# Kernel tuning notes

Hardware: AMD Instinct MI355X
Metric: run time of the kernel (lower is better)

Reference implementation:

```python
import jax, jax.numpy as jnp
import numpy as np

EMBED_DIM = 1024
N_HEADS = 16
HEAD_DIM = EMBED_DIM // N_HEADS
B, N = 4, 2048


def setup_inputs() -> dict:
    key = jax.random.key(0)
    k1, k2, k3, k4, k5 = jax.random.split(key, 5)
    x = jax.random.normal(k1, (B, N, EMBED_DIM), dtype=jnp.float32)
    # Per-head kqv Linear weights stacked: torch Linear(embed_dim, 3*head_dim)
    # torch stores weight as [out, in]; we store transposed [in, out] per head.
    scale = 1.0 / np.sqrt(EMBED_DIM)
    W_kqv = jax.random.uniform(k2, (N_HEADS, EMBED_DIM, 3 * HEAD_DIM), dtype=jnp.float32, minval=-scale, maxval=scale)
    b_kqv = jax.random.uniform(k3, (N_HEADS, 3 * HEAD_DIM), dtype=jnp.float32, minval=-scale, maxval=scale)
    W_proj = jax.random.uniform(k4, (EMBED_DIM, EMBED_DIM), dtype=jnp.float32, minval=-scale, maxval=scale)
    b_proj = jax.random.uniform(k5, (EMBED_DIM,), dtype=jnp.float32, minval=-scale, maxval=scale)
    return {"x": x, "W_kqv": W_kqv, "b_kqv": b_kqv, "W_proj": W_proj, "b_proj": b_proj}


def reference(x, W_kqv, b_kqv, W_proj, b_proj):
    Bx, Nx, D = x.shape
    H = W_kqv.shape[0]
    hd = W_kqv.shape[2] // 3
    # All per-head kqv projections at once: [B, H, N, 3*hd]
    kqv = jnp.einsum('bnd,hde->bhne', x, W_kqv) + b_kqv[None, :, None, :]
    # chunk order in source is (k, q, v)
    k, q, v = jnp.split(kqv, 3, axis=-1)
    # scores scaled by sqrt(head_dim) (D1 in attention_scores is head dim)
    scores = jnp.einsum('bhqd,bhkd->bhqk', q, k) / jnp.sqrt(jnp.float32(hd))
    causal = jnp.tril(jnp.ones((Nx, Nx), dtype=bool))  # [N, N]
    scores = jnp.where(causal[None, None, :, :], scores, -jnp.inf)
    attn = jax.nn.softmax(scores, axis=-1)
    sa = jnp.einsum('bhqk,bhkd->bhqd', attn, v)  # [B, H, N, hd]
    # concat heads along feature dim (head order preserved)
    sa = sa.transpose(0, 2, 1, 3).reshape(Bx, Nx, H * hd)
    # output projection: torch Linear with weight [out, in] -> y = sa @ W^T + b;
    # here W_proj is stored as [in, out]
    return sa @ W_proj + b_proj
```

## Files before the change

### kernel.cpp

```cpp
#include <hip/hip_runtime.h>
#include <math.h>

#define EMBED   1024
#define NHEADS  16
#define HD      64
#define BATCH   4
#define SEQ     2048
#define MROWS   (BATCH*SEQ)
#define NKV     8388608ull

typedef short short8 __attribute__((ext_vector_type(8)));
typedef float floatx4 __attribute__((ext_vector_type(4)));

__device__ __forceinline__ unsigned short f2b(float f) {
    union { float f; unsigned u; } v; v.f = f;
    unsigned r = v.u + 0x7FFFu + ((v.u >> 16) & 1u);
    return (unsigned short)(r >> 16);
}
__device__ __forceinline__ unsigned short f2b_fast(float f) {
    union { float f; unsigned u; } v; v.f = f;
    return (unsigned short)((v.u + 0x8000u) >> 16);
}

#define GLDS16(gp, lp) __builtin_amdgcn_global_load_lds( \
    (const __attribute__((address_space(1))) unsigned int*)(gp), \
    (__attribute__((address_space(3))) unsigned int*)(lp), 16, 0, 0)

__global__ __launch_bounds__(256) void convert_x(
    const float* __restrict__ x, unsigned short* __restrict__ x16)
{
    size_t idx = ((size_t)blockIdx.x * 256 + threadIdx.x) * 8;
    float4 a = *(const float4*)(x + idx);
    float4 b = *(const float4*)(x + idx + 4);
    ushort4 u0, u1;
    u0.x = f2b(a.x); u0.y = f2b(a.y); u0.z = f2b(a.z); u0.w = f2b(a.w);
    u1.x = f2b(b.x); u1.y = f2b(b.y); u1.z = f2b(b.z); u1.w = f2b(b.w);
    *(ushort4*)(x16 + idx) = u0;
    *(ushort4*)(x16 + idx + 4) = u1;
}

__global__ __launch_bounds__(256) void prep_wkqv(
    const float* __restrict__ Wk, unsigned short* __restrict__ Wt)
{
    __shared__ float tile[32][33];
    const int h = blockIdx.z;
    const int k0 = blockIdx.x * 32, e0 = blockIdx.y * 32;
    const float* inh = Wk + (size_t)h * 1024 * 192;
    const int tx = threadIdx.x & 31, ty = threadIdx.x >> 5;
    #pragma unroll
    for (int i = 0; i < 4; i++)
        tile[ty + i * 8][tx] = inh[(size_t)(k0 + ty + i * 8) * 192 + e0 + tx];
    __syncthreads();
    #pragma unroll
    for (int i = 0; i < 4; i++) {
        int e = e0 + ty + i * 8;
        int cp = (e >> 6) * 1024 + h * 64 + (e & 63);
        Wt[(size_t)cp * 1024 + k0 + tx] = f2b(tile[tx][ty + i * 8]);
    }
}

__global__ __launch_bounds__(256) void transpose_w(
    const float* __restrict__ in, unsigned short* __restrict__ outp, int R, int C)
{
    __shared__ float tile[32][33];
    const int r0 = blockIdx.x * 32, c0 = blockIdx.y * 32;
    const int tx = threadIdx.x & 31, ty = threadIdx.x >> 5;
    #pragma unroll
    for (int i = 0; i < 4; i++)
        tile[ty + i * 8][tx] = in[(size_t)(r0 + ty + i * 8) * C + c0 + tx];
    __syncthreads();
    #pragma unroll
    for (int i = 0; i < 4; i++)
        outp[(size_t)(c0 + ty + i * 8) * R + r0 + tx] = f2b(tile[tx][ty + i * 8]);
}

__global__ __launch_bounds__(512, 2) void gemm_kqv(
    const unsigned short* __restrict__ A,
    const unsigned short* __restrict__ Bt,
    const float* __restrict__ bk,
    unsigned short* __restrict__ Kb16,
    unsigned short* __restrict__ Qb16,
    unsigned short* __restrict__ Vt16)
{
    __shared__ unsigned short smem[65536];

    const int mt = blockIdx.x;
    const int ct = blockIdx.y;
    const int t = threadIdx.x;
    const int wave = t >> 6, lane = t & 63;
    const int lr = lane & 15, quad = lane >> 4;
    const int wr = wave >> 2, wc = wave & 3;
    const int row0 = mt * 256, col0 = ct * 256;
    const int swz8 = ((lane & 7) ^ ((lane >> 3) & 7)) * 8;
    const int c0 = ((quad) ^ (lr & 7)) * 8;
    const int c1 = ((4 + quad) ^ (lr & 7)) * 8;

    floatx4 acc[8][4];
    #pragma unroll
    for (int m = 0; m < 8; m++)
        #pragma unroll
        for (int n = 0; n < 4; n++) acc[m][n] = (floatx4){0.f, 0.f, 0.f, 0.f};

#define STG(G, R0, KC, L) do { \
    _Pragma("unroll") \
    for (int i_ = 0; i_ < 2; i_++) { \
        int rl_ = i_ * 64 + wave * 8 + (lane >> 3); \
        GLDS16((G) + (size_t)((R0) + rl_) * 1024 + (KC) + swz8, \
               (L) + rl_ * 64 + (lane & 7) * 8); \
    } } while (0)

    STG(A,  row0,       0,  smem);
    STG(A,  row0 + 128, 0,  smem + 8192);
    STG(Bt, col0,       0,  smem + 16384);
    STG(Bt, col0 + 128, 0,  smem + 16384 + 8192);
    STG(Bt, col0,       64, smem + 32768 + 16384);
    STG(Bt, col0 + 128, 64, smem + 32768 + 16384 + 8192);
    asm volatile("s_waitcnt vmcnt(4)" ::: "memory");
    __builtin_amdgcn_s_barrier();

    #pragma unroll 2
    for (int j = 0; j < 16; ++j) {
        unsigned short* Ab = smem + (j & 1) * 32768;
        unsigned short* Bb = Ab + 16384;
        unsigned short* An = smem + ((j + 1) & 1) * 32768;
        const unsigned short* pA = Ab + (wr * 128 + lr) * 64;
        const unsigned short* pB = Bb + (wc * 64 + lr) * 64;

        short8 b0[4], b1[4];

        {
            short8 af[4];
            #pragma unroll
            for (int m = 0; m < 4; m++) af[m] = *(const short8*)(pA + m * 1024 + c0);
            #pragma unroll
            for (int n = 0; n < 4; n++) b0[n] = *(const short8*)(pB + n * 1024 + c0);
            if (j < 15) STG(A, row0, (j + 1) * 64, An);
            __builtin_amdgcn_s_barrier();
            asm volatile("s_waitcnt lgkmcnt(0)" ::: "memory");
            __builtin_amdgcn_s_setprio(1);
            #pragma unroll
            for (int m = 0; m < 4; m++)
                #pragma unroll
                for (int n = 0; n < 4; n++)
                    acc[m][n] = __builtin_amdgcn_mfma_f32_16x16x32_bf16(af[m], b0[n], acc[m][n], 0, 0, 0);
            __builtin_amdgcn_s_setprio(0);
            __builtin_amdgcn_s_barrier();
        }
        {
            short8 af[4];
            #pragma unroll
            for (int m = 0; m < 4; m++) af[m] = *(const short8*)(pA + (m + 4) * 1024 + c0);
            #pragma unroll
            for (int n = 0; n < 4; n++) b1[n] = *(const short8*)(pB + n * 1024 + c1);
            if (j < 15) STG(A, row0 + 128, (j + 1) * 64, An + 8192);
            __builtin_amdgcn_s_barrier();
            asm volatile("s_waitcnt lgkmcnt(0)" ::: "memory");
            __builtin_amdgcn_s_setprio(1);
            #pragma unroll
            for (int m = 0; m < 4; m++)
                #pragma unroll
                for (int n = 0; n < 4; n++)
                    acc[m + 4][n] = __builtin_amdgcn_mfma_f32_16x16x32_bf16(af[m], b0[n], acc[m + 4][n], 0, 0, 0);
            __builtin_amdgcn_s_setprio(0);
            __builtin_amdgcn_s_barrier();
        }
        {
            short8 af[4];
            #pragma unroll
            for (int m = 0; m < 4; m++) af[m] = *(const short8*)(pA + m * 1024 + c1);
            if (j < 14) STG(Bt, col0, (j + 2) * 64, Bb);
            __builtin_amdgcn_s_barrier();
            asm volatile("s_waitcnt lgkmcnt(0)" ::: "memory");
            __builtin_amdgcn_s_setprio(1);
            #pragma unroll
            for (int m = 0; m < 4; m++)
                #pragma unroll
                for (int n = 0; n < 4; n++)
                    acc[m][n] = __builtin_amdgcn_mfma_f32_16x16x32_bf16(af[m], b1[n], acc[m][n], 0, 0, 0);
            __builtin_amdgcn_s_setprio(0);
            __builtin_amdgcn_s_barrier();
        }
        {
            short8 af[4];
            #pragma unroll
            for (int m = 0; m < 4; m++) af[m] = *(const short8*)(pA + (m + 4) * 1024 + c1);
            if (j < 14) STG(Bt, col0 + 128, (j + 2) * 64, Bb + 8192);
            __builtin_amdgcn_s_barrier();
            asm volatile("s_waitcnt lgkmcnt(0)" ::: "memory");
            __builtin_amdgcn_s_setprio(1);
            #pragma unroll
            for (int m = 0; m < 4; m++)
                #pragma unroll
                for (int n = 0; n < 4; n++)
                    acc[m + 4][n] = __builtin_amdgcn_mfma_f32_16x16x32_bf16(af[m], b1[n], acc[m + 4][n], 0, 0, 0);
            __builtin_amdgcn_s_setprio(0);
            if (j < 14)       asm volatile("s_waitcnt vmcnt(4)" ::: "memory");
            else if (j == 14) asm volatile("s_waitcnt vmcnt(0)" ::: "memory");
            __builtin_amdgcn_s_barrier();
        }
    }
#undef STG

    unsigned short* W = smem + wave * 8192;
    const int sec = ct >> 2;
    const int h = ((ct & 3) << 2) + wc;
    const int bidx = mt >> 3;
    const int rbase = ((mt * 256) & 2047) + wr * 128;

    float bias[4];
    #pragma unroll
    for (int n = 0; n < 4; n++) bias[n] = bk[h * 192 + sec * 64 + n * 16 + lr];

    if (sec < 2) {
        const float scl = (sec == 1) ? (0.125f * 1.44269504089f) : 1.0f;
        #pragma unroll
        for (int m = 0; m < 8; m++)
            #pragma unroll
            for (int n = 0; n < 4; n++) {
                int es = (n * 16 + lr) ^ (quad << 4);
                #pragma unroll
                for (int r = 0; r < 4; r++)
                    W[(m * 16 + quad * 4 + r) * 64 + es] = f2b((acc[m][n][r] + bias[n]) * scl);
            }
        __syncthreads();
        unsigned short* dst = ((sec == 0) ? Kb16 : Qb16)
                              + ((size_t)(bidx * 16 + h) * 2048 + rbase) * 64;
        const int rrow = lane >> 3, chunk = lane & 7;
        #pragma unroll
        for (int p = 0; p < 16; p++) {
            int row = p * 8 + rrow;
            int ch = chunk ^ (((row >> 2) & 3) << 1);
            *(float4*)(dst + (size_t)row * 64 + chunk * 8) =
                *(const float4*)(W + row * 64 + ch * 8);
        }
    } else {
        #pragma unroll
        for (int m = 0; m < 8; m++)
            #pragma unroll
            for (int n = 0; n < 4; n++) {
                int e = n * 16 + lr;
                ushort4 pk;
                pk.x = f2b(acc[m][n][0] + bias[n]);
                pk.y = f2b(acc[m][n][1] + bias[n]);
                pk.z = f2b(acc[m][n][2] + bias[n]);
                pk.w = f2b(acc[m][n][3] + bias[n]);
                int mp = m ^ (lr & 7);
                *(ushort4*)(W + e * 128 + mp * 16 + quad * 4) = pk;
            }
        __syncthreads();
        unsigned short* dstV = Vt16 + (size_t)(bidx * 16 + h) * 64 * 2048 + rbase;
        const int ev = lane >> 4, chunkR = lane & 15;
        #pragma unroll
        for (int p = 0; p < 16; p++) {
            int e = p * 4 + ev;
            int ch = chunkR ^ ((e & 7) << 1);
            *(float4*)(dstV + (size_t)e * 2048 + chunkR * 8) =
                *(const float4*)(W + e * 128 + ch * 8);
        }
    }
}

__global__ __launch_bounds__(256, 2) void attn_mfma(
    const unsigned short* __restrict__ Kb,
    const unsigned short* __restrict__ Qb,
    const unsigned short* __restrict__ Vt,
    unsigned short* __restrict__ sa)
{
    const int bx = blockIdx.x;
    const int bh = blockIdx.y;
    const int b = bh >> 4, h = bh & 15;
    const int wave = threadIdx.x >> 6;
    const int lane = threadIdx.x & 63;
    const int lr = lane & 15, quad = lane >> 4;
    const int qt_[2] = {bx, 15 - bx};

    __shared__ unsigned short Ks[64 * 64];
    __shared__ unsigned short Vs[64 * 64];
    __shared__ unsigned short Ps[4][2][16 * 72];

    const unsigned short* Kbh = Kb + (size_t)bh * 2048 * 64;
    const unsigned short* Vbh = Vt + (size_t)bh * 64 * 2048;
    const unsigned short* Qbh = Qb + (size_t)bh * 2048 * 64;

    short8 qf[2][2][2];
    #pragma unroll
    for (int tt = 0; tt < 2; tt++)
        #pragma unroll
        for (int s = 0; s < 2; s++) {
            const unsigned short* qp = Qbh +
                (size_t)(qt_[tt] * 128 + wave * 32 + s * 16 + lr) * 64 + quad * 8;
            qf[tt][s][0] = *(const short8*)(qp);
            qf[tt][s][1] = *(const short8*)(qp + 32);
        }

    floatx4 O[2][2][4];
    float ls[2][2][4];
    #pragma unroll
    for (int tt = 0; tt < 2; tt++)
        #pragma unroll
        for (int s = 0; s < 2; s++) {
            #pragma unroll
            for (int d = 0; d < 4; d++) O[tt][s][d] = (floatx4){0.f, 0.f, 0.f, 0.f};
            #pragma unroll
            for (int r = 0; r < 4; r++) ls[tt][s][r] = 0.f;
        }

    const int r_local = lane >> 3, cc = lane & 7;
    const int swz = cc ^ r_local;
    const int whalf = wave >> 1;

    const int ktmax = 2 * qt_[1] + 1;
    for (int kt = 0; kt <= ktmax; kt++) {
        const int k0 = kt * 64;
        __syncthreads();
        #pragma unroll
        for (int j = 0; j < 2; j++) {
            int R = wave * 16 + j * 8 + r_local;
            GLDS16(Kbh + (size_t)(k0 + R) * 64 + swz * 8, Ks + (wave * 16 + j * 8) * 64 + lane * 8);
            GLDS16(Vbh + (size_t)R * 2048 + k0 + swz * 8, Vs + (wave * 16 + j * 8) * 64 + lane * 8);
        }
        __syncthreads();

        #pragma unroll
        for (int tt = 0; tt < 2; tt++) {
            const int qt2 = qt_[tt];
            const int lim = 2 * qt2 + whalf;
            if (kt > lim) continue;

            floatx4 S[2][4];
            #pragma unroll
            for (int s = 0; s < 2; s++)
                #pragma unroll
                for (int a = 0; a < 4; a++) S[s][a] = (floatx4){0.f, 0.f, 0.f, 0.f};
            #pragma unroll
            for (int c = 0; c < 2; c++)
                #pragma unroll
                for (int a = 0; a < 4; a++) {
                    int R = a * 16 + lr;
                    short8 kf = *(const short8*)(Ks + R * 64 + (((c * 4 + quad) ^ (lr & 7)) * 8));
                    #pragma unroll
                    for (int s = 0; s < 2; s++)
                        S[s][a] = __builtin_amdgcn_mfma_f32_16x16x32_bf16(qf[tt][s][c], kf, S[s][a], 0, 0, 0);
                }

            if (kt == lim) {
                #pragma unroll
                for (int s = 0; s < 2; s++)
                    #pragma unroll
                    for (int a = 0; a < 4; a++) {
                        int col = k0 + a * 16 + lr;
                        #pragma unroll
                        for (int r = 0; r < 4; r++) {
                            int grow = qt2 * 128 + wave * 32 + s * 16 + quad * 4 + r;
                            if (col > grow) S[s][a][r] = -INFINITY;
                        }
                    }
            }

            #pragma unroll
            for (int s = 0; s < 2; s++)
                #pragma unroll
                for (int a = 0; a < 4; a++)
                    #pragma unroll
                    for (int r = 0; r < 4; r++) {
                        float p = __builtin_amdgcn_exp2f(S[s][a][r]);
                        ls[tt][s][r] += p;
                        Ps[wave][s][(quad * 4 + r) * 72 + a * 16 + lr] = f2b_fast(p);
                    }

            short8 pa[2][2];
            #pragma unroll
            for (int s = 0; s < 2; s++)
                #pragma unroll
                for (int c = 0; c < 2; c++)
                    pa[s][c] = *(const short8*)(Ps[wave][s] + lr * 72 + c * 32 + quad * 8);

            #pragma unroll
            for (int c = 0; c < 2; c++)
                #pragma unroll
                for (int d = 0; d < 4; d++) {
                    int R = d * 16 + lr;
                    short8 vf = *(const short8*)(Vs + R * 64 + (((c * 4 + quad) ^ (lr & 7)) * 8));
                    #pragma unroll
                    for (int s = 0; s < 2; s++)
                        O[tt][s][d] = __builtin_amdgcn_mfma_f32_16x16x32_bf16(pa[s][c], vf, O[tt][s][d], 0, 0, 0);
                }
        }
    }

    #pragma unroll
    for (int tt = 0; tt < 2; tt++)
        #pragma unroll
        for (int s = 0; s < 2; s++)
            #pragma unroll
            for (int r = 0; r < 4; r++) {
                float sm = ls[tt][s][r];
                sm += __shfl_xor(sm, 1);
                sm += __shfl_xor(sm, 2);
                sm += __shfl_xor(sm, 4);
                sm += __shfl_xor(sm, 8);
                float inv = 1.0f / sm;
                size_t base = ((size_t)(b * 2048 + qt_[tt] * 128 + wave * 32 + s * 16 + quad * 4 + r)) * 1024
                              + h * 64 + lr;
                #pragma unroll
                for (int d = 0; d < 4; d++)
                    sa[base + d * 16] = f2b(O[tt][s][d][r] * inv);
            }
}

__global__ __launch_bounds__(256) void gemm_proj(
    const unsigned short* __restrict__ A,
    const unsigned short* __restrict__ Bt,
    const float* __restrict__ bp,
    float* __restrict__ out)
{
    __shared__ unsigned short smem[16384];
    unsigned short* As = smem;
    unsigned short* Bs = smem + 8192;

    const int mt = blockIdx.x;
    const int ct = blockIdx.y;
    const int t = threadIdx.x;
    const int wave = t >> 6, lane = t & 63;
    const int lr = lane & 15, quad = lane >> 4;
    const int wm = wave >> 1, wn = wave & 1;
    const int row0 = mt * 128, col0 = ct * 128;
    const int sr = lane >> 3, sc = lane & 7;

    floatx4 acc[4][4];
    #pragma unroll
    for (int a = 0; a < 4; a++)
        #pragma unroll
        for (int n = 0; n < 4; n++) acc[a][n] = (floatx4){0.f, 0.f, 0.f, 0.f};

    for (int k0 = 0; k0 < 1024; k0 += 64) {
        __syncthreads();
        #pragma unroll
        for (int i = 0; i < 4; i++) {
            int q = wave + i * 4;
            GLDS16(A  + (size_t)(row0 + q * 8 + sr) * 1024 + k0 + sc * 8, As + q * 512);
            GLDS16(Bt + (size_t)(col0 + q * 8 + sr) * 1024 + k0 + sc * 8, Bs + q * 512);
        }
        __syncthreads();
        #pragma unroll
        for (int kc = 0; kc < 2; kc++) {
            short8 af[4], bf[4];
            #pragma unroll
            for (int i = 0; i < 4; i++) {
                af[i] = *(const short8*)(As + (wm * 64 + i * 16 + lr) * 64 + kc * 32 + quad * 8);
                bf[i] = *(const short8*)(Bs + (wn * 64 + i * 16 + lr) * 64 + kc * 32 + quad * 8);
            }
            #pragma unroll
            for (int a = 0; a < 4; a++)
                #pragma unroll
                for (int n = 0; n < 4; n++)
                    acc[a][n] = __builtin_amdgcn_mfma_f32_16x16x32_bf16(af[a], bf[n], acc[a][n], 0, 0, 0);
        }
    }

    float bias[4]; int cols[4];
    #pragma unroll
    for (int n = 0; n < 4; n++) {
        cols[n] = col0 + wn * 64 + n * 16 + lr;
        bias[n] = bp[cols[n]];
    }
    #pragma unroll
    for (int a = 0; a < 4; a++) {
        #pragma unroll
        for (int n = 0; n < 4; n++) {
            #pragma unroll
            for (int r = 0; r < 4; r++) {
                int m = row0 + wm * 64 + a * 16 + quad * 4 + r;
                out[(size_t)m * 1024 + cols[n]] = acc[a][n][r] + bias[n];
            }
        }
    }
}

extern "C" void kernel_launch(void* const* d_in, const int* in_sizes, int n_in,
                              void* d_out, int out_size, void* d_ws, size_t ws_size,
                              hipStream_t stream) {
    const float* x  = (const float*)d_in[0];
    const float* Wk = (const float*)d_in[1];
    const float* bk = (const float*)d_in[2];
    const float* Wp = (const float*)d_in[3];
    const float* bp = (const float*)d_in[4];
    float* out = (float*)d_out;

    unsigned short* Kb16 = (unsigned short*)d_ws;
    unsigned short* Qb16 = Kb16 + NKV;
    unsigned short* Vt16 = Qb16 + NKV;
    unsigned short* sa16 = Vt16 + NKV;
    unsigned short* x16  = sa16 + 8388608ull;
    unsigned short* Wt   = x16  + 8388608ull;
    unsigned short* Wpt  = Wt   + 3145728ull;

    convert_x<<<4096, 256, 0, stream>>>(x, x16);
    prep_wkqv<<<dim3(32, 6, 16), 256, 0, stream>>>(Wk, Wt);
    transpose_w<<<dim3(32, 32, 1), 256, 0, stream>>>(Wp, Wpt, 1024, 1024);
    gemm_kqv<<<dim3(32, 12), 512, 0, stream>>>(x16, Wt, bk, Kb16, Qb16, Vt16);
    attn_mfma<<<dim3(8, 64), 256, 0, stream>>>(Kb16, Qb16, Vt16, sa16);
    gemm_proj<<<dim3(64, 8), 256, 0, stream>>>(sa16, Wpt, bp, out);
}
```

Before: 254.1 us.

## Share pipelined 128x256 GEMM mainloop between KQV and output projection

Factors a swizzled, double-buffered 128x256 bf16 MFMA mainloop into a shared device function. gemm_kqv switches from 256x256 tiles to 128x256 tiles, doubling its grid from 384 to 768 blocks, which should fill the compute units more evenly. gemm_proj drops its simple single-buffered 128x128 loop for the pipelined 128x256 loop with 512 threads. The trade-off is less reuse of each B tile per block in gemm_kqv, and gemm_proj now has only 256 blocks.

```diff
diff --git a/kernel.cpp b/kernel.cpp
--- a/kernel.cpp
+++ b/kernel.cpp
@@ -74,6 +74,91 @@
         outp[(size_t)(c0 + ty + i * 8) * R + r0 + tx] = f2b(tile[tx][ty + i * 8]);
 }
 
+__device__ __forceinline__ void mainloop_128x256(
+    const unsigned short* __restrict__ Ag,
+    const unsigned short* __restrict__ Bg,
+    unsigned short* smem,
+    int row0, int col0, floatx4 (&acc)[4][4])
+{
+    const int t = threadIdx.x;
+    const int wave = t >> 6, lane = t & 63;
+    const int lr = lane & 15, quad = lane >> 4;
+    const int wr = wave >> 2, wc = wave & 3;
+    const int swz8 = ((lane & 7) ^ ((lane >> 3) & 7)) * 8;
+    const int c0 = (quad ^ (lr & 7)) * 8;
+    const int c1 = ((4 + quad) ^ (lr & 7)) * 8;
+
+    #pragma unroll
+    for (int m = 0; m < 4; m++)
+        #pragma unroll
+        for (int n = 0; n < 4; n++) acc[m][n] = (floatx4){0.f, 0.f, 0.f, 0.f};
+
+#define STG(G, R0, KC, L) do { \
+    _Pragma("unroll") \
+    for (int i_ = 0; i_ < 2; i_++) { \
+        int rl_ = i_ * 64 + wave * 8 + (lane >> 3); \
+        GLDS16((G) + (size_t)((R0) + rl_) * 1024 + (KC) + swz8, \
+               (L) + rl_ * 64 + (lane & 7) * 8); \
+    } } while (0)
+
+    STG(Ag, row0,       0,  smem);
+    STG(Bg, col0,       0,  smem + 8192);
+    STG(Bg, col0 + 128, 0,  smem + 16384);
+    STG(Bg, col0,       64, smem + 24576 + 8192);
+    STG(Bg, col0 + 128, 64, smem + 24576 + 16384);
+    asm volatile("s_waitcnt vmcnt(4)" ::: "memory");
+    __builtin_amdgcn_s_barrier();
+
+    #pragma unroll 2
+    for (int j = 0; j < 16; ++j) {
+        unsigned short* Ab = smem + (j & 1) * 24576;
+        unsigned short* Bb = Ab + 8192;
+        unsigned short* An = smem + ((j + 1) & 1) * 24576;
+        const unsigned short* pA = Ab + (wr * 64 + lr) * 64;
+        const unsigned short* pB = Bb + (wc * 64 + lr) * 64;
+
+        short8 af0[4], af1[4], b0[4], b1[4];
+
+        #pragma unroll
+        for (int m = 0; m < 4; m++) af0[m] = *(const short8*)(pA + m * 1024 + c0);
+        #pragma unroll
+        for (int n = 0; n < 4; n++) b0[n] = *(const short8*)(pB + n * 1024 + c0);
+        #pragma unroll
+        for (int n = 0; n < 4; n++) b1[n] = *(const short8*)(pB + n * 1024 + c1);
+        if (j < 15) STG(Ag, row0, (j + 1) * 64, An);
+        __builtin_amdgcn_s_barrier();
+        asm volatile("s_waitcnt lgkmcnt(0)" ::: "memory");
+        __builtin_amdgcn_s_setprio(1);
+        #pragma unroll
+        for (int m = 0; m < 4; m++)
+            #pragma unroll
+            for (int n = 0; n < 4; n++)
+                acc[m][n] = __builtin_amdgcn_mfma_f32_16x16x32_bf16(af0[m], b0[n], acc[m][n], 0, 0, 0);
+        __builtin_amdgcn_s_setprio(0);
+        __builtin_amdgcn_s_barrier();
+
+        #pragma unroll
+        for (int m = 0; m < 4; m++) af1[m] = *(const short8*)(pA + m * 1024 + c1);
+        if (j < 14) {
+            STG(Bg, col0,       (j + 2) * 64, Bb);
+            STG(Bg, col0 + 128, (j + 2) * 64, Bb + 8192);
+        }
+        __builtin_amdgcn_s_barrier();
+        asm volatile("s_waitcnt lgkmcnt(0)" ::: "memory");
+        __builtin_amdgcn_s_setprio(1);
+        #pragma unroll
+        for (int m = 0; m < 4; m++)
+            #pragma unroll
+            for (int n = 0; n < 4; n++)
+                acc[m][n] = __builtin_amdgcn_mfma_f32_16x16x32_bf16(af1[m], b1[n], acc[m][n], 0, 0, 0);
+        __builtin_amdgcn_s_setprio(0);
+        if (j < 14)       asm volatile("s_waitcnt vmcnt(4)" ::: "memory");
+        else if (j == 14) asm volatile("s_waitcnt vmcnt(0)" ::: "memory");
+        __builtin_amdgcn_s_barrier();
+    }
+#undef STG
+}
+
 __global__ __launch_bounds__(512, 2) void gemm_kqv(
     const unsigned short* __restrict__ A,
     const unsigned short* __restrict__ Bt,
@@ -82,130 +167,25 @@
     unsigned short* __restrict__ Qb16,
     unsigned short* __restrict__ Vt16)
 {
-    __shared__ unsigned short smem[65536];
+    __shared__ unsigned short smem[49152];
 
     const int mt = blockIdx.x;
     const int ct = blockIdx.y;
+    const int row0 = mt * 128, col0 = ct * 256;
+
+    floatx4 acc[4][4];
+    mainloop_128x256(A, Bt, smem, row0, col0, acc);
+
     const int t = threadIdx.x;
     const int wave = t >> 6, lane = t & 63;
     const int lr = lane & 15, quad = lane >> 4;
     const int wr = wave >> 2, wc = wave & 3;
-    const int row0 = mt * 256, col0 = ct * 256;
-    const int swz8 = ((lane & 7) ^ ((lane >> 3) & 7)) * 8;
-    const int c0 = ((quad) ^ (lr & 7)) * 8;
-    const int c1 = ((4 + quad) ^ (lr & 7)) * 8;
-
-    floatx4 acc[8][4];
-    #pragma unroll
-    for (int m = 0; m < 8; m++)
-        #pragma unroll
-        for (int n = 0; n < 4; n++) acc[m][n] = (floatx4){0.f, 0.f, 0.f, 0.f};
-
-#define STG(G, R0, KC, L) do { \
-    _Pragma("unroll") \
-    for (int i_ = 0; i_ < 2; i_++) { \
-        int rl_ = i_ * 64 + wave * 8 + (lane >> 3); \
-        GLDS16((G) + (size_t)((R0) + rl_) * 1024 + (KC) + swz8, \
-               (L) + rl_ * 64 + (lane & 7) * 8); \
-    } } while (0)
-
-    STG(A,  row0,       0,  smem);
-    STG(A,  row0 + 128, 0,  smem + 8192);
-    STG(Bt, col0,       0,  smem + 16384);
-    STG(Bt, col0 + 128, 0,  smem + 16384 + 8192);
-    STG(Bt, col0,       64, smem + 32768 + 16384);
-    STG(Bt, col0 + 128, 64, smem + 32768 + 16384 + 8192);
-    asm volatile("s_waitcnt vmcnt(4)" ::: "memory");
-    __builtin_amdgcn_s_barrier();
-
-    #pragma unroll 2
-    for (int j = 0; j < 16; ++j) {
-        unsigned short* Ab = smem + (j & 1) * 32768;
-        unsigned short* Bb = Ab + 16384;
-        unsigned short* An = smem + ((j + 1) & 1) * 32768;
-        const unsigned short* pA = Ab + (wr * 128 + lr) * 64;
-        const unsigned short* pB = Bb + (wc * 64 + lr) * 64;
-
-        short8 b0[4], b1[4];
-
-        {
-            short8 af[4];
-            #pragma unroll
-            for (int m = 0; m < 4; m++) af[m] = *(const short8*)(pA + m * 1024 + c0);
-            #pragma unroll
-            for (int n = 0; n < 4; n++) b0[n] = *(const short8*)(pB + n * 1024 + c0);
-            if (j < 15) STG(A, row0, (j + 1) * 64, An);
-            __builtin_amdgcn_s_barrier();
-            asm volatile("s_waitcnt lgkmcnt(0)" ::: "memory");
-            __builtin_amdgcn_s_setprio(1);
-            #pragma unroll
-            for (int m = 0; m < 4; m++)
-                #pragma unroll
-                for (int n = 0; n < 4; n++)
-                    acc[m][n] = __builtin_amdgcn_mfma_f32_16x16x32_bf16(af[m], b0[n], acc[m][n], 0, 0, 0);
-            __builtin_amdgcn_s_setprio(0);
-            __builtin_amdgcn_s_barrier();
-        }
-        {
-            short8 af[4];
-            #pragma unroll
-            for (int m = 0; m < 4; m++) af[m] = *(const short8*)(pA + (m + 4) * 1024 + c0);
-            #pragma unroll
-            for (int n = 0; n < 4; n++) b1[n] = *(const short8*)(pB + n * 1024 + c1);
-            if (j < 15) STG(A, row0 + 128, (j + 1) * 64, An + 8192);
-            __builtin_amdgcn_s_barrier();
-            asm volatile("s_waitcnt lgkmcnt(0)" ::: "memory");
-            __builtin_amdgcn_s_setprio(1);
-            #pragma unroll
-            for (int m = 0; m < 4; m++)
-                #pragma unroll
-                for (int n = 0; n < 4; n++)
-                    acc[m + 4][n] = __builtin_amdgcn_mfma_f32_16x16x32_bf16(af[m], b0[n], acc[m + 4][n], 0, 0, 0);
-            __builtin_amdgcn_s_setprio(0);
-            __builtin_amdgcn_s_barrier();
-        }
-        {
-            short8 af[4];
-            #pragma unroll
-            for (int m = 0; m < 4; m++) af[m] = *(const short8*)(pA + m * 1024 + c1);
-            if (j < 14) STG(Bt, col0, (j + 2) * 64, Bb);
-            __builtin_amdgcn_s_barrier();
-            asm volatile("s_waitcnt lgkmcnt(0)" ::: "memory");
-            __builtin_amdgcn_s_setprio(1);
-            #pragma unroll
-            for (int m = 0; m < 4; m++)
-                #pragma unroll
-                for (int n = 0; n < 4; n++)
-                    acc[m][n] = __builtin_amdgcn_mfma_f32_16x16x32_bf16(af[m], b1[n], acc[m][n], 0, 0, 0);
-            __builtin_amdgcn_s_setprio(0);
-            __builtin_amdgcn_s_barrier();
-        }
-        {
-            short8 af[4];
-            #pragma unroll
-            for (int m = 0; m < 4; m++) af[m] = *(const short8*)(pA + (m + 4) * 1024 + c1);
-            if (j < 14) STG(Bt, col0 + 128, (j + 2) * 64, Bb + 8192);
-            __builtin_amdgcn_s_barrier();
-            asm volatile("s_waitcnt lgkmcnt(0)" ::: "memory");
-            __builtin_amdgcn_s_setprio(1);
-            #pragma unroll
-            for (int m = 0; m < 4; m++)
-                #pragma unroll
-                for (int n = 0; n < 4; n++)
-                    acc[m + 4][n] = __builtin_amdgcn_mfma_f32_16x16x32_bf16(af[m], b1[n], acc[m + 4][n], 0, 0, 0);
-            __builtin_amdgcn_s_setprio(0);
-            if (j < 14)       asm volatile("s_waitcnt vmcnt(4)" ::: "memory");
-            else if (j == 14) asm volatile("s_waitcnt vmcnt(0)" ::: "memory");
-            __builtin_amdgcn_s_barrier();
-        }
-    }
-#undef STG
-
-    unsigned short* W = smem + wave * 8192;
+
+    unsigned short* W = smem + wave * 4096;
     const int sec = ct >> 2;
     const int h = ((ct & 3) << 2) + wc;
-    const int bidx = mt >> 3;
-    const int rbase = ((mt * 256) & 2047) + wr * 128;
+    const int bidx = row0 >> 11;
+    const int rbase = (row0 & 2047) + wr * 64;
 
     float bias[4];
     #pragma unroll
@@ -214,7 +194,7 @@
     if (sec < 2) {
         const float scl = (sec == 1) ? (0.125f * 1.44269504089f) : 1.0f;
         #pragma unroll
-        for (int m = 0; m < 8; m++)
+        for (int m = 0; m < 4; m++)
             #pragma unroll
             for (int n = 0; n < 4; n++) {
                 int es = (n * 16 + lr) ^ (quad << 4);
@@ -227,7 +207,7 @@
                               + ((size_t)(bidx * 16 + h) * 2048 + rbase) * 64;
         const int rrow = lane >> 3, chunk = lane & 7;
         #pragma unroll
-        for (int p = 0; p < 16; p++) {
+        for (int p = 0; p < 8; p++) {
             int row = p * 8 + rrow;
             int ch = chunk ^ (((row >> 2) & 3) << 1);
             *(float4*)(dst + (size_t)row * 64 + chunk * 8) =
@@ -235,7 +215,7 @@
         }
     } else {
         #pragma unroll
-        for (int m = 0; m < 8; m++)
+        for (int m = 0; m < 4; m++)
             #pragma unroll
             for (int n = 0; n < 4; n++) {
                 int e = n * 16 + lr;
@@ -244,18 +224,18 @@
                 pk.y = f2b(acc[m][n][1] + bias[n]);
                 pk.z = f2b(acc[m][n][2] + bias[n]);
                 pk.w = f2b(acc[m][n][3] + bias[n]);
-                int mp = m ^ (lr & 7);
-                *(ushort4*)(W + e * 128 + mp * 16 + quad * 4) = pk;
+                int mp = m ^ (lr & 3);
+                *(ushort4*)(W + e * 64 + mp * 16 + quad * 4) = pk;
             }
         __syncthreads();
         unsigned short* dstV = Vt16 + (size_t)(bidx * 16 + h) * 64 * 2048 + rbase;
-        const int ev = lane >> 4, chunkR = lane & 15;
-        #pragma unroll
-        for (int p = 0; p < 16; p++) {
-            int e = p * 4 + ev;
-            int ch = chunkR ^ ((e & 7) << 1);
+        const int ev = lane >> 3, chunkR = lane & 7;
+        #pragma unroll
+        for (int p = 0; p < 8; p++) {
+            int e = p * 8 + ev;
+            int ch = chunkR ^ ((e & 3) << 1);
             *(float4*)(dstV + (size_t)e * 2048 + chunkR * 8) =
-                *(const float4*)(W + e * 128 + ch * 8);
+                *(const float4*)(W + e * 64 + ch * 8);
         }
     }
 }
@@ -408,60 +388,30 @@
             }
 }
 
-__global__ __launch_bounds__(256) void gemm_proj(
+__global__ __launch_bounds__(512, 2) void gemm_proj(
     const unsigned short* __restrict__ A,
     const unsigned short* __restrict__ Bt,
     const float* __restrict__ bp,
     float* __restrict__ out)
 {
-    __shared__ unsigned short smem[16384];
-    unsigned short* As = smem;
-    unsigned short* Bs = smem + 8192;
+    __shared__ unsigned short smem[49152];
 
     const int mt = blockIdx.x;
     const int ct = blockIdx.y;
+    const int row0 = mt * 128, col0 = ct * 256;
+
+    floatx4 acc[4][4];
+    mainloop_128x256(A, Bt, smem, row0, col0, acc);
+
     const int t = threadIdx.x;
-    const int wave = t >> 6, lane = t & 63;
+    const int lane = t & 63, wave = t >> 6;
     const int lr = lane & 15, quad = lane >> 4;
-    const int wm = wave >> 1, wn = wave & 1;
-    const int row0 = mt * 128, col0 = ct * 128;
-    const int sr = lane >> 3, sc = lane & 7;
-
-    floatx4 acc[4][4];
-    #pragma unroll
-    for (int a = 0; a < 4; a++)
-        #pragma unroll
-        for (int n = 0; n < 4; n++) acc[a][n] = (floatx4){0.f, 0.f, 0.f, 0.f};
-
-    for (int k0 = 0; k0 < 1024; k0 += 64) {
-        __syncthreads();
-        #pragma unroll
-        for (int i = 0; i < 4; i++) {
-            int q = wave + i * 4;
-            GLDS16(A  + (size_t)(row0 + q * 8 + sr) * 1024 + k0 + sc * 8, As + q * 512);
-            GLDS16(Bt + (size_t)(col0 + q * 8 + sr) * 1024 + k0 + sc * 8, Bs + q * 512);
-        }
-        __syncthreads();
-        #pragma unroll
-        for (int kc = 0; kc < 2; kc++) {
-            short8 af[4], bf[4];
-            #pragma unroll
-            for (int i = 0; i < 4; i++) {
-                af[i] = *(const short8*)(As + (wm * 64 + i * 16 + lr) * 64 + kc * 32 + quad * 8);
-                bf[i] = *(const short8*)(Bs + (wn * 64 + i * 16 + lr) * 64 + kc * 32 + quad * 8);
-            }
-            #pragma unroll
-            for (int a = 0; a < 4; a++)
-                #pragma unroll
-                for (int n = 0; n < 4; n++)
-                    acc[a][n] = __builtin_amdgcn_mfma_f32_16x16x32_bf16(af[a], bf[n], acc[a][n], 0, 0, 0);
-        }
-    }
+    const int wr = wave >> 2, wc = wave & 3;
 
     float bias[4]; int cols[4];
     #pragma unroll
     for (int n = 0; n < 4; n++) {
-        cols[n] = col0 + wn * 64 + n * 16 + lr;
+        cols[n] = col0 + wc * 64 + n * 16 + lr;
         bias[n] = bp[cols[n]];
     }
     #pragma unroll
@@ -470,7 +420,7 @@
         for (int n = 0; n < 4; n++) {
             #pragma unroll
             for (int r = 0; r < 4; r++) {
-                int m = row0 + wm * 64 + a * 16 + quad * 4 + r;
+                int m = row0 + wr * 64 + a * 16 + quad * 4 + r;
                 out[(size_t)m * 1024 + cols[n]] = acc[a][n][r] + bias[n];
             }
         }
@@ -498,7 +448,7 @@
     convert_x<<<4096, 256, 0, stream>>>(x, x16);
     prep_wkqv<<<dim3(32, 6, 16), 256, 0, stream>>>(Wk, Wt);
     transpose_w<<<dim3(32, 32, 1), 256, 0, stream>>>(Wp, Wpt, 1024, 1024);
-    gemm_kqv<<<dim3(32, 12), 512, 0, stream>>>(x16, Wt, bk, Kb16, Qb16, Vt16);
+    gemm_kqv<<<dim3(64, 12), 512, 0, stream>>>(x16, Wt, bk, Kb16, Qb16, Vt16);
     attn_mfma<<<dim3(8, 64), 256, 0, stream>>>(Kb16, Qb16, Vt16, sa16);
-    gemm_proj<<<dim3(64, 8), 256, 0, stream>>>(sa16, Wpt, bp, out);
-}
+    gemm_proj<<<dim3(64, 4), 512, 0, stream>>>(sa16, Wpt, bp, out);
+}
```

New measurement: 245.4 us. 1.04x faster.
